# Performance work log

Measured on AMD Instinct MI355X. Metric: run time of the kernel, lower is better.

## Reference

```python
import jax, jax.numpy as jnp
import numpy as np

D_SUMMARY = 128
N_LAYERS = 24
N_HEADS = 16
D_HEAD = 64
HIDDEN = 512
ACTIVE_MIN = 12
ROT = 16
THETA = 10000.0
B, P = 16, 128
L_ACT = N_LAYERS - ACTIVE_MIN
OUT_DIM = N_HEADS * 2 * D_HEAD


def setup_inputs() -> dict:
    key = jax.random.key(0)
    k1, k2, k3, k4, k5, k6 = jax.random.split(key, 6)
    summary_stack = jax.random.normal(k1, (B, P, D_SUMMARY), jnp.float32)
    positions = jnp.sort(jax.random.randint(k2, (P,), 0, 8192))
    s1 = 1.0 / np.sqrt(D_SUMMARY)
    s2 = 1.0 / np.sqrt(HIDDEN)
    W1 = jax.random.uniform(k3, (L_ACT, D_SUMMARY, HIDDEN), jnp.float32, -s1, s1)
    b1 = jax.random.uniform(k4, (L_ACT, HIDDEN), jnp.float32, -s1, s1)
    W2 = jax.random.uniform(k5, (L_ACT, HIDDEN, OUT_DIM), jnp.float32, -s2, s2)
    b2 = jax.random.uniform(k6, (L_ACT, OUT_DIM), jnp.float32, -s2, s2)
    return {"summary_stack": summary_stack, "positions": positions,
            "W1": W1, "b1": b1, "W2": W2, "b2": b2}


def reference(summary_stack, positions, W1, b1, W2, b2):
    # Batched 2-layer MLP across all active layers (grouped GEMM)
    h = jax.nn.relu(jnp.einsum('bps,lsh->lbph', summary_stack, W1) + b1[:, None, None, :])
    kv = jnp.einsum('lbph,lho->lbpo', h, W2) + b2[:, None, None, :]
    kv = kv.reshape(L_ACT, B, P, N_HEADS, 2, D_HEAD)
    k = jnp.transpose(kv[..., 0, :], (0, 1, 3, 2, 4))  # (L,B,H,P,D)
    v = jnp.transpose(kv[..., 1, :], (0, 1, 3, 2, 4))
    # RoPE on first ROT dims of K
    inv_freq = 1.0 / (THETA ** (jnp.arange(0, ROT, 2, dtype=jnp.float32) / ROT))
    freqs = positions.astype(jnp.float32)[:, None] * inv_freq[None, :]  # (P, ROT//2)
    emb = jnp.concatenate([freqs, freqs], axis=-1)  # (P, ROT)
    cos, sin = jnp.cos(emb), jnp.sin(emb)
    k_rot, k_pass = k[..., :ROT], k[..., ROT:]
    rot_half = jnp.concatenate([-k_rot[..., ROT // 2:], k_rot[..., :ROT // 2]], axis=-1)
    k_emb = k_rot * cos + rot_half * sin
    k = jnp.concatenate([k_emb, k_pass], axis=-1)
    # Inactive layers get zero K/V
    zeros = jnp.zeros((ACTIVE_MIN, B, N_HEADS, P, D_HEAD), k.dtype)
    k_all = jnp.concatenate([zeros, k], axis=0)
    v_all = jnp.concatenate([zeros, v], axis=0)
    return jnp.stack([k_all, v_all], axis=1)  # (n_layers, 2, B, H, P, D)
```

## Files before the change

### kernel.cpp

```cpp
#include <hip/hip_runtime.h>
#include <hip/hip_bf16.h>

#define L_ACT   12
#define BDIM    16
#define PDIM    128
#define DSUM    128
#define HID     512
#define ODIM    2048
#define NHEAD   16
#define DHEAD   64
#define MROWS   2048

typedef short short8 __attribute__((ext_vector_type(8)));
typedef float f32x4  __attribute__((ext_vector_type(4)));

__device__ __forceinline__ void gload_lds16(const __hip_bfloat16* g, __hip_bfloat16* l) {
  __builtin_amdgcn_global_load_lds(
      (const __attribute__((address_space(1))) unsigned int*)g,
      (__attribute__((address_space(3))) unsigned int*)l, 16, 0, 0);
}

__global__ __launch_bounds__(256) void zerofill_kernel(f32x4* __restrict__ p, int n16) {
  int stride = gridDim.x * 256;
  for (int i = blockIdx.x * 256 + threadIdx.x; i < n16; i += stride)
    p[i] = {0.f, 0.f, 0.f, 0.f};
}

__global__ __launch_bounds__(256) void prep_small(
    const float* __restrict__ summary, const int* __restrict__ positions,
    const float* __restrict__ W1,
    __hip_bfloat16* __restrict__ A_bf, float* __restrict__ cs,
    __hip_bfloat16* __restrict__ W1T) {
  const int bid = blockIdx.x;
  const int tid = threadIdx.x;
  if (bid < 1024) {
    int i = bid * 256 + tid;
    A_bf[i] = __float2bfloat16(summary[i]);
    if (i < PDIM * 8) {
      int p = i >> 3, f = i & 7;
      double inv = pow(10000.0, -(double)f / 8.0);
      double ang = (double)positions[p] * inv;
      cs[i]        = (float)cos(ang);
      cs[1024 + i] = (float)sin(ang);
    }
  } else {
    __shared__ float t[32][33];
    int idx = bid - 1024;
    int bx = idx & 15, by = (idx >> 4) & 3, l = idx >> 6;
    int o0 = bx * 32, j0 = by * 32;
    int tx = tid & 31, ty = tid >> 5;
    const float* ip = W1 + (size_t)l * DSUM * HID;
#pragma unroll
    for (int r = 0; r < 32; r += 8)
      t[ty + r][tx] = ip[(size_t)(j0 + ty + r) * HID + o0 + tx];
    __syncthreads();
    __hip_bfloat16* op = W1T + (size_t)l * DSUM * HID;
#pragma unroll
    for (int r = 0; r < 32; r += 8)
      op[(size_t)(o0 + ty + r) * DSUM + j0 + tx] = __float2bfloat16(t[tx][ty + r]);
  }
}

__global__ __launch_bounds__(256) void gemm1_128(
    const __hip_bfloat16* __restrict__ Aall,
    const __hip_bfloat16* __restrict__ Ball,
    const float* __restrict__ bias,
    __hip_bfloat16* __restrict__ Hall,
    const float* __restrict__ W2,
    __hip_bfloat16* __restrict__ W2T,
    f32x4* __restrict__ zeroBase, int doZero) {
  const int KTOT = DSUM, NTOT = HID;
  __shared__ __hip_bfloat16 ldsA[128 * 64];
  __shared__ __hip_bfloat16 ldsB[128 * 64];
  const int l    = blockIdx.z;
  const int n0   = blockIdx.x * 128;
  const int m0   = blockIdx.y * 128;
  const int tid  = threadIdx.x;
  const int wid  = tid >> 6;
  const int lane = tid & 63;
  const int wr = wid >> 1, wc = wid & 1;
  const __hip_bfloat16* A  = Aall;
  const __hip_bfloat16* Bt = Ball + (size_t)l * NTOT * KTOT;

  f32x4 acc[4][4];
#pragma unroll
  for (int m = 0; m < 4; ++m)
#pragma unroll
    for (int n = 0; n < 4; ++n)
      acc[m][n] = {0.f, 0.f, 0.f, 0.f};

  const int srowi = lane >> 3;
  const int sblk  = (lane & 7) ^ srowi;

  for (int kt = 0; kt < KTOT / 64; ++kt) {
    __syncthreads();
#pragma unroll
    for (int s = 0; s < 4; ++s) {
      int seg = wid * 4 + s;
      int row = seg * 8 + srowi;
      gload_lds16(A  + (size_t)(m0 + row) * KTOT + kt * 64 + sblk * 8, ldsA + seg * 512);
      gload_lds16(Bt + (size_t)(n0 + row) * KTOT + kt * 64 + sblk * 8, ldsB + seg * 512);
    }
    __syncthreads();
#pragma unroll
    for (int kk = 0; kk < 2; ++kk) {
      short8 af[4], bfr[4];
#pragma unroll
      for (int m = 0; m < 4; ++m) {
        int row = wr * 64 + m * 16 + (lane & 15);
        int off = (kk * 64 + (lane >> 4) * 16) ^ ((row & 7) << 4);
        af[m] = *(const short8*)((const char*)ldsA + row * 128 + off);
      }
#pragma unroll
      for (int n = 0; n < 4; ++n) {
        int row = wc * 64 + n * 16 + (lane & 15);
        int off = (kk * 64 + (lane >> 4) * 16) ^ ((row & 7) << 4);
        bfr[n] = *(const short8*)((const char*)ldsB + row * 128 + off);
      }
#pragma unroll
      for (int m = 0; m < 4; ++m)
#pragma unroll
        for (int n = 0; n < 4; ++n)
          acc[m][n] = __builtin_amdgcn_mfma_f32_16x16x32_bf16(af[m], bfr[n], acc[m][n], 0, 0, 0);
    }
  }

  const int bid = blockIdx.x + 4 * blockIdx.y + 64 * blockIdx.z;

  if (doZero) {
    const f32x4 z = {0.f, 0.f, 0.f, 0.f};
    f32x4* zp = zeroBase + (size_t)bid * 16384;
#pragma unroll
    for (int i = 0; i < 64; ++i)
      __builtin_nontemporal_store(z, zp + i * 256 + tid);
  }

  const int colBase = n0 + wc * 64 + (lane & 15);
  const int rowBase = m0 + wr * 64 + ((lane >> 4) << 2);
  __hip_bfloat16* H = Hall + (size_t)l * MROWS * HID;
#pragma unroll
  for (int n = 0; n < 4; ++n) {
    int col = colBase + n * 16;
    float bb = bias[l * NTOT + col];
#pragma unroll
    for (int m = 0; m < 4; ++m) {
      int row = rowBase + m * 16;
#pragma unroll
      for (int j = 0; j < 4; ++j) {
        float v = acc[m][n][j] + bb;
        v = v > 0.f ? v : 0.f;
        H[(size_t)(row + j) * HID + col] = __float2bfloat16(v);
      }
    }
  }

  {
    float* tb = (float*)ldsA;
    const int tx = tid & 31, ty = tid >> 5;
    const int tbase = bid * 16;
#pragma unroll 1
    for (int tt = 0; tt < 16; ++tt) {
      int t = tbase + tt;
      int lz = t >> 10, rem = t & 1023;
      int jt = rem >> 6, ot = rem & 63;
      int j0 = jt * 32, o0 = ot * 32;
      const float* ip = W2 + (size_t)lz * HID * ODIM;
      __hip_bfloat16* op = W2T + (size_t)lz * HID * ODIM;
      __syncthreads();
#pragma unroll
      for (int r = 0; r < 32; r += 8)
        tb[(ty + r) * 33 + tx] = ip[(size_t)(j0 + ty + r) * ODIM + o0 + tx];
      __syncthreads();
#pragma unroll
      for (int r = 0; r < 32; r += 8)
        op[(size_t)(o0 + ty + r) * HID + j0 + tx] = __float2bfloat16(tb[tx * 33 + ty + r]);
    }
  }
}

__global__ __launch_bounds__(512, 1) void gemm2_pipe(
    const __hip_bfloat16* __restrict__ Aall,
    const __hip_bfloat16* __restrict__ Ball,
    const float* __restrict__ bias,
    const float* __restrict__ cs,
    float* __restrict__ O) {
  __shared__ __hip_bfloat16 lds[4 * 16384];
  const int orig = blockIdx.x + 8 * blockIdx.y + 64 * blockIdx.z;
  const int nw   = (orig & 7) * 96 + (orig >> 3);
  const int bx   = nw & 7;
  const int by   = (nw >> 3) & 7;
  const int l    = nw >> 6;
  const int n0  = bx * 256;
  const int m0  = by * 256;
  const int tid = threadIdx.x;
  const int wid = tid >> 6, lane = tid & 63;
  const int wm  = wid >> 2, wn = wid & 3;
  const __hip_bfloat16* A  = Aall + (size_t)l * MROWS * HID;
  const __hip_bfloat16* Bt = Ball + (size_t)l * ODIM * HID;

  f32x4 acc[8][4];
#pragma unroll
  for (int m = 0; m < 8; ++m)
#pragma unroll
    for (int n = 0; n < 4; ++n)
      acc[m][n] = {0.f, 0.f, 0.f, 0.f};

  const int cidx0 = wid * 128 + lane;
  const int cidx1 = cidx0 + 64;
  const int r0 = cidx0 >> 2, c0 = (cidx0 & 3) ^ ((r0 >> 1) & 3);
  const int r1 = cidx1 >> 2, c1 = (cidx1 & 3) ^ ((r1 >> 1) & 3);

#define STAGE_A(slot, kt) do {                                                      \
    gload_lds16(A + (size_t)(m0 + r0) * HID + (kt) * 32 + c0 * 8,                   \
                lds + (slot) * 16384 + wid * 1024);                                 \
    gload_lds16(A + (size_t)(m0 + r1) * HID + (kt) * 32 + c1 * 8,                   \
                lds + (slot) * 16384 + wid * 1024 + 512);                           \
  } while (0)
#define STAGE_B(slot, kt) do {                                                      \
    gload_lds16(Bt + (size_t)(n0 + r0) * HID + (kt) * 32 + c0 * 8,                  \
                lds + (slot) * 16384 + 8192 + wid * 1024);                          \
    gload_lds16(Bt + (size_t)(n0 + r1) * HID + (kt) * 32 + c1 * 8,                  \
                lds + (slot) * 16384 + 8192 + wid * 1024 + 512);                    \
  } while (0)

  const int kq   = lane >> 4;
  const int rl15 = lane & 15;

#define LD_FRAG(dst, base, rr) do {                                                 \
    int r_ = (rr);                                                                  \
    int off_ = r_ * 64 + ((kq ^ ((r_ >> 1) & 3)) << 4);                             \
    dst = *(const short8*)((const char*)(base) + off_);                             \
  } while (0)

  STAGE_A(0, 0); STAGE_B(0, 0);
  STAGE_A(1, 1); STAGE_B(1, 1);
  STAGE_A(2, 2); STAGE_B(2, 2);
  asm volatile("s_waitcnt vmcnt(8)" ::: "memory");
  __builtin_amdgcn_s_barrier();

  const int NT = HID / 32;
  for (int t = 0; t < NT; ++t) {
    const __hip_bfloat16* sa = lds + (t & 3) * 16384;
    const __hip_bfloat16* sb = sa + 8192;
    short8 af[4], bfr[4];

#pragma unroll
    for (int n = 0; n < 4; ++n) LD_FRAG(bfr[n], sb, wn * 64 + n * 16 + rl15);
#pragma unroll
    for (int mi = 0; mi < 4; ++mi) LD_FRAG(af[mi], sa, wm * 128 + mi * 16 + rl15);
    if (t + 3 < NT) STAGE_A((t + 3) & 3, t + 3);
    __builtin_amdgcn_s_barrier();
    __builtin_amdgcn_s_setprio(1);
#pragma unroll
    for (int mi = 0; mi < 4; ++mi)
#pragma unroll
      for (int n = 0; n < 4; ++n)
        acc[mi][n] = __builtin_amdgcn_mfma_f32_16x16x32_bf16(af[mi], bfr[n], acc[mi][n], 0, 0, 0);
    __builtin_amdgcn_s_setprio(0);
    __builtin_amdgcn_s_barrier();

#pragma unroll
    for (int mi = 0; mi < 4; ++mi) LD_FRAG(af[mi], sa, wm * 128 + 64 + mi * 16 + rl15);
    if (t + 3 < NT) STAGE_B((t + 3) & 3, t + 3);
    __builtin_amdgcn_s_barrier();
    __builtin_amdgcn_s_setprio(1);
#pragma unroll
    for (int mi = 0; mi < 4; ++mi)
#pragma unroll
      for (int n = 0; n < 4; ++n)
        acc[4 + mi][n] = __builtin_amdgcn_mfma_f32_16x16x32_bf16(af[mi], bfr[n], acc[4 + mi][n], 0, 0, 0);
    __builtin_amdgcn_s_setprio(0);
    if (t < NT - 1) {
      if (t <= NT - 4)      asm volatile("s_waitcnt vmcnt(8)" ::: "memory");
      else if (t == NT - 3) asm volatile("s_waitcnt vmcnt(4)" ::: "memory");
      else                  asm volatile("s_waitcnt vmcnt(0)" ::: "memory");
    }
    __builtin_amdgcn_s_barrier();
  }
#undef STAGE_A
#undef STAGE_B
#undef LD_FRAG

  __syncthreads();
  const int head = bx * 2 + (wn >> 1);
  const int tkv  = wn & 1;
  const int bidx = by * 2 + wm;
  float* slab = O + ((((size_t)(l + L_ACT) * 2 + tkv) * BDIM + bidx) * NHEAD + head) * (PDIM * DHEAD);
  const bool ropeWave = (tkv == 0);

  float bb[4];
#pragma unroll
  for (int n = 0; n < 4; ++n) bb[n] = bias[l * ODIM + n0 + wn * 64 + n * 16 + rl15];

  float* Tw = (float*)lds + wid * 2080;

#pragma unroll
  for (int c = 0; c < 4; ++c) {
#pragma unroll
    for (int mh = 0; mh < 2; ++mh) {
      int mf = c * 2 + mh;
      int pl = mh * 16 + (lane >> 4) * 4;
#pragma unroll
      for (int n = 0; n < 4; ++n) {
#pragma unroll
        for (int j = 0; j < 4; ++j) {
          float v = acc[mf][n][j] + bb[n];
          if (ropeWave && n == 0) {
            float partner = __shfl_xor(v, 8);
            int p = c * 32 + pl + j;
            float cv = cs[p * 8 + (lane & 7)];
            float sv = cs[1024 + p * 8 + (lane & 7)];
            v = v * cv + (((lane & 15) < 8) ? -partner : partner) * sv;
          }
          Tw[(pl + j) * 65 + n * 16 + rl15] = v;
        }
      }
    }
#pragma unroll
    for (int it = 0; it < 8; ++it) {
      int pl = it * 4 + (lane >> 4);
      f32x4 vv = *(const f32x4*)(Tw + pl * 65 + rl15 * 4);
      __builtin_nontemporal_store(vv, (f32x4*)(slab + (size_t)(c * 32 + pl) * DHEAD + rl15 * 4));
    }
  }
}

extern "C" void kernel_launch(void* const* d_in, const int* in_sizes, int n_in,
                              void* d_out, int out_size, void* d_ws, size_t ws_size,
                              hipStream_t stream) {
  const float* summary   = (const float*)d_in[0];
  const int*   positions = (const int*)d_in[1];
  const float* W1 = (const float*)d_in[2];
  const float* b1 = (const float*)d_in[3];
  const float* W2 = (const float*)d_in[4];
  const float* b2 = (const float*)d_in[5];
  float* out = (float*)d_out;

  const size_t SCRATCH_BYTES = 52436992;
  const bool useWs = (ws_size >= SCRATCH_BYTES);
  char* sc = useWs ? (char*)d_ws : (char*)d_out;
  __hip_bfloat16* h_bf = (__hip_bfloat16*)sc;
  __hip_bfloat16* W2T  = (__hip_bfloat16*)(sc + 25165824);
  __hip_bfloat16* W1T  = (__hip_bfloat16*)(sc + 50331648);
  __hip_bfloat16* A_bf = (__hip_bfloat16*)(sc + 51904512);
  float*          cs   = (float*)(sc + 52428800);

  prep_small<<<1792, 256, 0, stream>>>(summary, positions, W1, A_bf, cs, W1T);

  gemm1_128<<<dim3(HID / 128, MROWS / 128, L_ACT), 256, 0, stream>>>(
      A_bf, W1T, b1, h_bf, W2, W2T, (f32x4*)d_out, useWs ? 1 : 0);
  gemm2_pipe<<<dim3(ODIM / 256, MROWS / 256, L_ACT), 512, 0, stream>>>(h_bf, W2T, b2, cs, out);

  if (!useWs)
    zerofill_kernel<<<2048, 256, 0, stream>>>((f32x4*)d_out, 12582912);
}
```

Measured before the change: 136.7 us.

## Fuse W2 transpose/convert into gemm2 loads and summary convert into gemm1

Removes the separate W2 fp32-to-bf16 transpose pass (previously done inside gemm1) and the summary bf16 conversion pass. gemm2 now loads fp32 W2 directly through registers, converts to bf16 and writes swizzled tiles to LDS, using a double-buffered B region and register prefetch two stages ahead. gemm1 converts fp32 summary rows to bf16 on the fly into LDS. This saves a full write and re-read of a bf16 copy of W2, but each of the 96 gemm2 blocks now reads fp32 W2 (8 row-tiles share each column slab), which doubles B traffic and adds register pressure and conversion ALU work in the main loop.

```diff
diff --git a/kernel.cpp b/kernel.cpp
--- a/kernel.cpp
+++ b/kernel.cpp
@@ -11,6 +11,7 @@
 #define DHEAD   64
 #define MROWS   2048
 
+typedef short s16x4  __attribute__((ext_vector_type(4)));
 typedef short short8 __attribute__((ext_vector_type(8)));
 typedef float f32x4  __attribute__((ext_vector_type(4)));
 
@@ -20,23 +21,26 @@
       (__attribute__((address_space(3))) unsigned int*)l, 16, 0, 0);
 }
 
+__device__ __forceinline__ short f2bf(float x) {
+  __hip_bfloat16 h = __float2bfloat16(x);
+  return *reinterpret_cast<short*>(&h);
+}
+
 __global__ __launch_bounds__(256) void zerofill_kernel(f32x4* __restrict__ p, int n16) {
   int stride = gridDim.x * 256;
   for (int i = blockIdx.x * 256 + threadIdx.x; i < n16; i += stride)
     p[i] = {0.f, 0.f, 0.f, 0.f};
 }
 
-__global__ __launch_bounds__(256) void prep_small(
-    const float* __restrict__ summary, const int* __restrict__ positions,
-    const float* __restrict__ W1,
-    __hip_bfloat16* __restrict__ A_bf, float* __restrict__ cs,
-    __hip_bfloat16* __restrict__ W1T) {
+__global__ __launch_bounds__(256) void prep_tiny(
+    const int* __restrict__ positions, const float* __restrict__ W1,
+    float* __restrict__ cs, __hip_bfloat16* __restrict__ W1T) {
   const int bid = blockIdx.x;
   const int tid = threadIdx.x;
-  if (bid < 1024) {
-    int i = bid * 256 + tid;
-    A_bf[i] = __float2bfloat16(summary[i]);
-    if (i < PDIM * 8) {
+  if (bid == 768) {
+#pragma unroll
+    for (int q = 0; q < 4; ++q) {
+      int i = q * 256 + tid;
       int p = i >> 3, f = i & 7;
       double inv = pow(10000.0, -(double)f / 8.0);
       double ang = (double)positions[p] * inv;
@@ -45,8 +49,7 @@
     }
   } else {
     __shared__ float t[32][33];
-    int idx = bid - 1024;
-    int bx = idx & 15, by = (idx >> 4) & 3, l = idx >> 6;
+    int bx = bid & 15, by = (bid >> 4) & 3, l = bid >> 6;
     int o0 = bx * 32, j0 = by * 32;
     int tx = tid & 31, ty = tid >> 5;
     const float* ip = W1 + (size_t)l * DSUM * HID;
@@ -62,12 +65,10 @@
 }
 
 __global__ __launch_bounds__(256) void gemm1_128(
-    const __hip_bfloat16* __restrict__ Aall,
+    const float* __restrict__ summary,
     const __hip_bfloat16* __restrict__ Ball,
     const float* __restrict__ bias,
     __hip_bfloat16* __restrict__ Hall,
-    const float* __restrict__ W2,
-    __hip_bfloat16* __restrict__ W2T,
     f32x4* __restrict__ zeroBase, int doZero) {
   const int KTOT = DSUM, NTOT = HID;
   __shared__ __hip_bfloat16 ldsA[128 * 64];
@@ -79,7 +80,6 @@
   const int wid  = tid >> 6;
   const int lane = tid & 63;
   const int wr = wid >> 1, wc = wid & 1;
-  const __hip_bfloat16* A  = Aall;
   const __hip_bfloat16* Bt = Ball + (size_t)l * NTOT * KTOT;
 
   f32x4 acc[4][4];
@@ -98,8 +98,17 @@
     for (int s = 0; s < 4; ++s) {
       int seg = wid * 4 + s;
       int row = seg * 8 + srowi;
-      gload_lds16(A  + (size_t)(m0 + row) * KTOT + kt * 64 + sblk * 8, ldsA + seg * 512);
       gload_lds16(Bt + (size_t)(n0 + row) * KTOT + kt * 64 + sblk * 8, ldsB + seg * 512);
+    }
+#pragma unroll
+    for (int j = 0; j < 8; ++j) {
+      int s = j * 256 + tid;
+      int r = s >> 4, g = s & 15;
+      f32x4 v = *(const f32x4*)(summary + (size_t)(m0 + r) * DSUM + kt * 64 + g * 4);
+      s16x4 w;
+      w[0] = f2bf(v[0]); w[1] = f2bf(v[1]); w[2] = f2bf(v[2]); w[3] = f2bf(v[3]);
+      int ch = g >> 1;
+      *(s16x4*)((char*)ldsA + r * 128 + ((ch ^ (r & 7)) << 4) + (g & 1) * 8) = w;
     }
     __syncthreads();
 #pragma unroll
@@ -153,50 +162,24 @@
       }
     }
   }
-
-  {
-    float* tb = (float*)ldsA;
-    const int tx = tid & 31, ty = tid >> 5;
-    const int tbase = bid * 16;
-#pragma unroll 1
-    for (int tt = 0; tt < 16; ++tt) {
-      int t = tbase + tt;
-      int lz = t >> 10, rem = t & 1023;
-      int jt = rem >> 6, ot = rem & 63;
-      int j0 = jt * 32, o0 = ot * 32;
-      const float* ip = W2 + (size_t)lz * HID * ODIM;
-      __hip_bfloat16* op = W2T + (size_t)lz * HID * ODIM;
-      __syncthreads();
-#pragma unroll
-      for (int r = 0; r < 32; r += 8)
-        tb[(ty + r) * 33 + tx] = ip[(size_t)(j0 + ty + r) * ODIM + o0 + tx];
-      __syncthreads();
-#pragma unroll
-      for (int r = 0; r < 32; r += 8)
-        op[(size_t)(o0 + ty + r) * HID + j0 + tx] = __float2bfloat16(tb[tx * 33 + ty + r]);
-    }
-  }
 }
 
 __global__ __launch_bounds__(512, 1) void gemm2_pipe(
     const __hip_bfloat16* __restrict__ Aall,
-    const __hip_bfloat16* __restrict__ Ball,
+    const float* __restrict__ W2,
     const float* __restrict__ bias,
     const float* __restrict__ cs,
     float* __restrict__ O) {
-  __shared__ __hip_bfloat16 lds[4 * 16384];
+  __shared__ __hip_bfloat16 lds[6 * 8192];
   const int orig = blockIdx.x + 8 * blockIdx.y + 64 * blockIdx.z;
   const int nw   = (orig & 7) * 96 + (orig >> 3);
-  const int bx   = nw & 7;
-  const int by   = (nw >> 3) & 7;
-  const int l    = nw >> 6;
-  const int n0  = bx * 256;
-  const int m0  = by * 256;
+  const int bx = nw & 7, by = (nw >> 3) & 7, l = nw >> 6;
+  const int n0 = bx * 256, m0 = by * 256;
   const int tid = threadIdx.x;
   const int wid = tid >> 6, lane = tid & 63;
   const int wm  = wid >> 2, wn = wid & 3;
-  const __hip_bfloat16* A  = Aall + (size_t)l * MROWS * HID;
-  const __hip_bfloat16* Bt = Ball + (size_t)l * ODIM * HID;
+  const __hip_bfloat16* A = Aall + (size_t)l * MROWS * HID;
+  const float* W2l = W2 + (size_t)l * HID * ODIM;
 
   f32x4 acc[8][4];
 #pragma unroll
@@ -212,15 +195,40 @@
 
 #define STAGE_A(slot, kt) do {                                                      \
     gload_lds16(A + (size_t)(m0 + r0) * HID + (kt) * 32 + c0 * 8,                   \
-                lds + (slot) * 16384 + wid * 1024);                                 \
+                lds + (slot) * 8192 + wid * 1024);                                  \
     gload_lds16(A + (size_t)(m0 + r1) * HID + (kt) * 32 + c1 * 8,                   \
-                lds + (slot) * 16384 + wid * 1024 + 512);                           \
-  } while (0)
-#define STAGE_B(slot, kt) do {                                                      \
-    gload_lds16(Bt + (size_t)(n0 + r0) * HID + (kt) * 32 + c0 * 8,                  \
-                lds + (slot) * 16384 + 8192 + wid * 1024);                          \
-    gload_lds16(Bt + (size_t)(n0 + r1) * HID + (kt) * 32 + c1 * 8,                  \
-                lds + (slot) * 16384 + 8192 + wid * 1024 + 512);                    \
+                lds + (slot) * 8192 + wid * 1024 + 512);                            \
+  } while (0)
+
+  const int bn = tid & 255;
+  const int bc = tid >> 8;
+  const int bswz0 = (bc     ) ^ ((bn >> 1) & 3);
+  const int bswz1 = (bc + 2 ) ^ ((bn >> 1) & 3);
+  const float* bsrc0 = W2l + (size_t)(bc * 8) * ODIM + n0 + bn;
+  const float* bsrc1 = bsrc0 + (size_t)16 * ODIM;
+
+  float b_a0, b_a1, b_a2, b_a3, b_a4, b_a5, b_a6, b_a7,
+        b_a8, b_a9, b_a10, b_a11, b_a12, b_a13, b_a14, b_a15;
+  float b_b0, b_b1, b_b2, b_b3, b_b4, b_b5, b_b6, b_b7,
+        b_b8, b_b9, b_b10, b_b11, b_b12, b_b13, b_b14, b_b15;
+
+#define BLOAD(P, kt) do {                                                           \
+    const float* p0_ = bsrc0 + (size_t)(kt) * 32 * ODIM;                            \
+    const float* p1_ = bsrc1 + (size_t)(kt) * 32 * ODIM;                            \
+    P##0 = p0_[0*ODIM]; P##1 = p0_[1*ODIM]; P##2 = p0_[2*ODIM]; P##3 = p0_[3*ODIM]; \
+    P##4 = p0_[4*ODIM]; P##5 = p0_[5*ODIM]; P##6 = p0_[6*ODIM]; P##7 = p0_[7*ODIM]; \
+    P##8 = p1_[0*ODIM]; P##9 = p1_[1*ODIM]; P##10 = p1_[2*ODIM]; P##11 = p1_[3*ODIM];\
+    P##12 = p1_[4*ODIM]; P##13 = p1_[5*ODIM]; P##14 = p1_[6*ODIM]; P##15 = p1_[7*ODIM];\
+  } while (0)
+
+#define BWRITE(P, bufbyte) do {                                                     \
+    short8 w0_, w1_;                                                                \
+    w0_[0] = f2bf(P##0); w0_[1] = f2bf(P##1); w0_[2] = f2bf(P##2); w0_[3] = f2bf(P##3);\
+    w0_[4] = f2bf(P##4); w0_[5] = f2bf(P##5); w0_[6] = f2bf(P##6); w0_[7] = f2bf(P##7);\
+    w1_[0] = f2bf(P##8); w1_[1] = f2bf(P##9); w1_[2] = f2bf(P##10); w1_[3] = f2bf(P##11);\
+    w1_[4] = f2bf(P##12); w1_[5] = f2bf(P##13); w1_[6] = f2bf(P##14); w1_[7] = f2bf(P##15);\
+    *(short8*)((bufbyte) + bn * 64 + bswz0 * 16) = w0_;                             \
+    *(short8*)((bufbyte) + bn * 64 + bswz1 * 16) = w1_;                             \
   } while (0)
 
   const int kq   = lane >> 4;
@@ -232,53 +240,64 @@
     dst = *(const short8*)((const char*)(base) + off_);                             \
   } while (0)
 
-  STAGE_A(0, 0); STAGE_B(0, 0);
-  STAGE_A(1, 1); STAGE_B(1, 1);
-  STAGE_A(2, 2); STAGE_B(2, 2);
-  asm volatile("s_waitcnt vmcnt(8)" ::: "memory");
+  BLOAD(b_a, 0);
+  __builtin_amdgcn_sched_barrier(0);
+  STAGE_A(0, 0); STAGE_A(1, 1); STAGE_A(2, 2);
+  __builtin_amdgcn_sched_barrier(0);
+  BWRITE(b_a, (char*)lds + 65536);
+  __builtin_amdgcn_sched_barrier(0);
+  BLOAD(b_b, 1);
+  __builtin_amdgcn_sched_barrier(0);
+  asm volatile("s_waitcnt vmcnt(16)" ::: "memory");
+  asm volatile("s_waitcnt lgkmcnt(0)" ::: "memory");
   __builtin_amdgcn_s_barrier();
 
-  const int NT = HID / 32;
-  for (int t = 0; t < NT; ++t) {
-    const __hip_bfloat16* sa = lds + (t & 3) * 16384;
-    const __hip_bfloat16* sb = sa + 8192;
-    short8 af[4], bfr[4];
-
-#pragma unroll
-    for (int n = 0; n < 4; ++n) LD_FRAG(bfr[n], sb, wn * 64 + n * 16 + rl15);
-#pragma unroll
-    for (int mi = 0; mi < 4; ++mi) LD_FRAG(af[mi], sa, wm * 128 + mi * 16 + rl15);
-    if (t + 3 < NT) STAGE_A((t + 3) & 3, t + 3);
-    __builtin_amdgcn_s_barrier();
-    __builtin_amdgcn_s_setprio(1);
-#pragma unroll
-    for (int mi = 0; mi < 4; ++mi)
-#pragma unroll
-      for (int n = 0; n < 4; ++n)
-        acc[mi][n] = __builtin_amdgcn_mfma_f32_16x16x32_bf16(af[mi], bfr[n], acc[mi][n], 0, 0, 0);
-    __builtin_amdgcn_s_setprio(0);
-    __builtin_amdgcn_s_barrier();
-
-#pragma unroll
-    for (int mi = 0; mi < 4; ++mi) LD_FRAG(af[mi], sa, wm * 128 + 64 + mi * 16 + rl15);
-    if (t + 3 < NT) STAGE_B((t + 3) & 3, t + 3);
-    __builtin_amdgcn_s_barrier();
-    __builtin_amdgcn_s_setprio(1);
-#pragma unroll
-    for (int mi = 0; mi < 4; ++mi)
-#pragma unroll
-      for (int n = 0; n < 4; ++n)
-        acc[4 + mi][n] = __builtin_amdgcn_mfma_f32_16x16x32_bf16(af[mi], bfr[n], acc[4 + mi][n], 0, 0, 0);
-    __builtin_amdgcn_s_setprio(0);
-    if (t < NT - 1) {
-      if (t <= NT - 4)      asm volatile("s_waitcnt vmcnt(8)" ::: "memory");
-      else if (t == NT - 3) asm volatile("s_waitcnt vmcnt(4)" ::: "memory");
-      else                  asm volatile("s_waitcnt vmcnt(0)" ::: "memory");
-    }
-    __builtin_amdgcn_s_barrier();
-  }
+#define ITER_BODY(T, PL, PW) do {                                                   \
+    const int t_ = (T);                                                             \
+    const char* sa_ = (const char*)lds + (t_ & 3) * 16384;                          \
+    const char* sb_ = (const char*)lds + 65536 + (t_ & 1) * 16384;                  \
+    short8 af[4], bfr[4];                                                           \
+    _Pragma("unroll")                                                               \
+    for (int n_ = 0; n_ < 4; ++n_) LD_FRAG(bfr[n_], sb_, wn * 64 + n_ * 16 + rl15); \
+    _Pragma("unroll")                                                               \
+    for (int mi_ = 0; mi_ < 4; ++mi_) LD_FRAG(af[mi_], sa_, wm * 128 + mi_ * 16 + rl15);\
+    if (t_ + 3 < 16) STAGE_A((t_ + 3) & 3, t_ + 3);                                 \
+    __builtin_amdgcn_sched_barrier(0);                                              \
+    if (t_ + 2 < 16) BLOAD(PL, t_ + 2);                                             \
+    __builtin_amdgcn_sched_barrier(0);                                              \
+    __builtin_amdgcn_s_barrier();                                                   \
+    __builtin_amdgcn_s_setprio(1);                                                  \
+    _Pragma("unroll")                                                               \
+    for (int mi_ = 0; mi_ < 4; ++mi_)                                               \
+      _Pragma("unroll")                                                             \
+      for (int n_ = 0; n_ < 4; ++n_)                                                \
+        acc[mi_][n_] = __builtin_amdgcn_mfma_f32_16x16x32_bf16(af[mi_], bfr[n_], acc[mi_][n_], 0, 0, 0);\
+    __builtin_amdgcn_s_setprio(0);                                                  \
+    _Pragma("unroll")                                                               \
+    for (int mi_ = 0; mi_ < 4; ++mi_) LD_FRAG(af[mi_], sa_, wm * 128 + 64 + mi_ * 16 + rl15);\
+    __builtin_amdgcn_s_setprio(1);                                                  \
+    _Pragma("unroll")                                                               \
+    for (int mi_ = 0; mi_ < 4; ++mi_)                                               \
+      _Pragma("unroll")                                                             \
+      for (int n_ = 0; n_ < 4; ++n_)                                                \
+        acc[4 + mi_][n_] = __builtin_amdgcn_mfma_f32_16x16x32_bf16(af[mi_], bfr[n_], acc[4 + mi_][n_], 0, 0, 0);\
+    __builtin_amdgcn_s_setprio(0);                                                  \
+    if (t_ + 1 < 16) {                                                              \
+      __builtin_amdgcn_sched_barrier(0);                                            \
+      BWRITE(PW, (char*)lds + 65536 + ((t_ + 1) & 1) * 16384);                      \
+      asm volatile("s_waitcnt lgkmcnt(0)" ::: "memory");                            \
+    }                                                                               \
+    __builtin_amdgcn_s_barrier();                                                   \
+  } while (0)
+
+  for (int t = 0; t < 16; t += 2) {
+    ITER_BODY(t,     b_a, b_b);
+    ITER_BODY(t + 1, b_b, b_a);
+  }
+#undef ITER_BODY
 #undef STAGE_A
-#undef STAGE_B
+#undef BLOAD
+#undef BWRITE
 #undef LD_FRAG
 
   __syncthreads();
@@ -336,20 +355,19 @@
   const float* b2 = (const float*)d_in[5];
   float* out = (float*)d_out;
 
-  const size_t SCRATCH_BYTES = 52436992;
+  const size_t SCRATCH_BYTES = 25165824 + 1572864 + 8192;
   const bool useWs = (ws_size >= SCRATCH_BYTES);
   char* sc = useWs ? (char*)d_ws : (char*)d_out;
   __hip_bfloat16* h_bf = (__hip_bfloat16*)sc;
-  __hip_bfloat16* W2T  = (__hip_bfloat16*)(sc + 25165824);
-  __hip_bfloat16* W1T  = (__hip_bfloat16*)(sc + 50331648);
-  __hip_bfloat16* A_bf = (__hip_bfloat16*)(sc + 51904512);
-  float*          cs   = (float*)(sc + 52428800);
-
-  prep_small<<<1792, 256, 0, stream>>>(summary, positions, W1, A_bf, cs, W1T);
+  __hip_bfloat16* W1T  = (__hip_bfloat16*)(sc + 25165824);
+  float*          cs   = (float*)(sc + 25165824 + 1572864);
+
+  prep_tiny<<<769, 256, 0, stream>>>(positions, W1, cs, W1T);
 
   gemm1_128<<<dim3(HID / 128, MROWS / 128, L_ACT), 256, 0, stream>>>(
-      A_bf, W1T, b1, h_bf, W2, W2T, (f32x4*)d_out, useWs ? 1 : 0);
-  gemm2_pipe<<<dim3(ODIM / 256, MROWS / 256, L_ACT), 512, 0, stream>>>(h_bf, W2T, b2, cs, out);
+      summary, W1T, b1, h_bf, (f32x4*)d_out, useWs ? 1 : 0);
+  gemm2_pipe<<<dim3(ODIM / 256, MROWS / 256, L_ACT), 512, 0, stream>>>(
+      h_bf, W2, b2, cs, out);
 
   if (!useWs)
     zerofill_kernel<<<2048, 256, 0, stream>>>((f32x4*)d_out, 12582912);
```

Measured after the change: 146.4 us. 1.07x slower.
